# Optimization experiments

Hardware: AMD Instinct MI355X
Metric: run time of the kernel (lower is better)

## Reference

```python
import jax, jax.numpy as jnp
import numpy as np
import math

B, S, H, NS = 64, 1024, 1024, 8
TEMPERATURE = 1.0


def setup_inputs() -> dict:
    key = jax.random.key(0)
    ks = jax.random.split(key, 14)
    sc = 1.0 / math.sqrt(H)
    inp = {
        "x": jax.random.normal(ks[0], (B, S, H), dtype=jnp.float32),
        "Wq": jax.random.normal(ks[1], (H, H), dtype=jnp.float32) * sc,
        "bq": jax.random.normal(ks[2], (H,), dtype=jnp.float32) * sc,
        "Wk": jax.random.normal(ks[3], (H, H), dtype=jnp.float32) * sc,
        "bk": jax.random.normal(ks[4], (H,), dtype=jnp.float32) * sc,
        "Wv": jax.random.normal(ks[5], (H, H), dtype=jnp.float32) * sc,
        "bv": jax.random.normal(ks[6], (H,), dtype=jnp.float32) * sc,
        "Wp": jax.random.normal(ks[7], (NS, H, H), dtype=jnp.float32) * sc,
        "bp": jax.random.normal(ks[8], (NS, H), dtype=jnp.float32) * sc,
        "Ws": jax.random.normal(ks[9], (H, NS), dtype=jnp.float32) * sc,
        "bs": jax.random.normal(ks[10], (NS,), dtype=jnp.float32) * sc,
        "Wo": jax.random.normal(ks[11], (H, H), dtype=jnp.float32) * sc,
        "bo": jax.random.normal(ks[12], (H,), dtype=jnp.float32) * sc,
    }
    return inp


def reference(x, Wq, bq, Wk, bk, Wv, bv, Wp, bp, Ws, bs, Wo, bo):
    b, s_len, h = x.shape
    ns = Wp.shape[0]
    inv_base = 1.0 / math.sqrt(h * TEMPERATURE)
    inv_h = 1.0 / math.sqrt(h)

    x_last = x[:, -1, :]                      # [B,H]
    q = x_last @ Wq + bq                      # [B,H]
    k = x @ Wk + bk                           # [B,S,H]
    v = x @ Wv + bv                           # [B,S,H]

    attn_base = jax.nn.softmax(jnp.einsum("bh,bsh->bs", q, k) * inv_base, axis=-1)
    base_context = jnp.einsum("bs,bsh->bh", attn_base, v)   # [B,H]

    scale_importance = jax.nn.softmax(x_last @ Ws + bs, axis=-1)  # [B,NS]

    combined = jnp.zeros((b, h), dtype=x.dtype)
    for i in range(ns):
        size = max(1, s_len // (2 ** i))
        if size == 1:
            pooled = jnp.mean(x, axis=1, keepdims=True)      # [B,1,H]
        else:
            stride = max(1, size // 2)
            # S divisible by stride; window j = halves j and j+1
            half_sums = x.reshape(b, s_len // stride, stride, h).sum(axis=2)
            pooled = (half_sums[:, :-1] + half_sums[:, 1:]) / size  # [B,nw,H]
        feat = jnp.tanh(pooled @ Wp[i] + bp[i])              # [B,nw,H]
        fa = jax.nn.softmax(jnp.einsum("bh,bnh->bn", q, feat) * inv_h, axis=-1)
        ctx = jnp.einsum("bn,bnh->bh", fa, feat)
        combined = combined + scale_importance[:, i:i + 1] * ctx

    return (base_context + combined) @ Wo + bo
```

## Files before the change

kernel.cpp:

```cpp
#include <hip/hip_runtime.h>
#include <cstdint>
#include <cstddef>

#define BB 64
#define SS 1024
#define HH 1024
#define NSS 8

__device__ __constant__ int PBrow_c[8]    = {0,128,384,896,1920,3968,8064,16256};
__device__ __constant__ int realbase_c[8] = {0,64,256,704,1664,3648,7680,15808};

#define INV32 0.03125f

typedef __attribute__((ext_vector_type(8))) short short8;
typedef __attribute__((ext_vector_type(4))) float f32x4;

__device__ __forceinline__ uint16_t f2bf(float f) {
  union { float f; uint32_t u; } v; v.f = f;
  uint32_t r = v.u + 0x7fffu + ((v.u >> 16) & 1u);
  return (uint16_t)(r >> 16);
}
__device__ __forceinline__ float bf_lo(uint32_t w) { return __uint_as_float(w << 16); }
__device__ __forceinline__ float bf_hi(uint32_t w) { return __uint_as_float(w & 0xffff0000u); }

__device__ __forceinline__ void gld_lds16(const void* g, void* l) {
  __builtin_amdgcn_global_load_lds((const __attribute__((address_space(1))) uint32_t*)g,
                                   (__attribute__((address_space(3))) uint32_t*)l, 16, 0, 0);
}

template<bool TRANSB>
__global__ __launch_bounds__(256) void gemm64(
    const float* __restrict__ A, size_t a_stride,
    const float* __restrict__ W,
    const float* __restrict__ bias,
    const float* __restrict__ addb,
    float* __restrict__ out)
{
  __shared__ float As[64][68];
  __shared__ float Bs[64][68];
  const int t  = threadIdx.x;
  const int nt = blockIdx.x;
  const int ks = blockIdx.y;
  const int m0 = (t >> 4) << 2;
  const int n0 = (t & 15) << 2;
  float acc[4][4] = {};
  for (int kt = 0; kt < 4; ++kt) {
    const int k0 = ks * 256 + kt * 64;
    {
      const int m  = t >> 2;
      const int kb = (t & 3) << 4;
      #pragma unroll
      for (int j = 0; j < 4; ++j) {
        const int k = kb + j * 4;
        const float4 v = *(const float4*)(A + (size_t)m * a_stride + k0 + k);
        As[k+0][m] = v.x; As[k+1][m] = v.y; As[k+2][m] = v.z; As[k+3][m] = v.w;
      }
    }
    if (!TRANSB) {
      const int k  = t >> 2;
      const int nb = (t & 3) << 4;
      #pragma unroll
      for (int j = 0; j < 4; ++j) {
        const int n = nb + j * 4;
        *(float4*)&Bs[k][n] = *(const float4*)(W + (size_t)(k0 + k) * HH + nt * 64 + n);
      }
    } else {
      const int n  = t >> 2;
      const int kb = (t & 3) << 4;
      #pragma unroll
      for (int j = 0; j < 4; ++j) {
        const int k = kb + j * 4;
        const float4 v = *(const float4*)(W + (size_t)(nt * 64 + n) * HH + k0 + k);
        Bs[k+0][n] = v.x; Bs[k+1][n] = v.y; Bs[k+2][n] = v.z; Bs[k+3][n] = v.w;
      }
    }
    __syncthreads();
    #pragma unroll 16
    for (int k = 0; k < 64; ++k) {
      const float4 av = *(const float4*)&As[k][m0];
      const float4 bv = *(const float4*)&Bs[k][n0];
      const float a[4] = {av.x, av.y, av.z, av.w};
      const float b[4] = {bv.x, bv.y, bv.z, bv.w};
      #pragma unroll
      for (int i2 = 0; i2 < 4; ++i2)
        #pragma unroll
        for (int j2 = 0; j2 < 4; ++j2)
          acc[i2][j2] += a[i2] * b[j2];
    }
    __syncthreads();
  }
  #pragma unroll
  for (int i2 = 0; i2 < 4; ++i2) {
    const int m = m0 + i2;
    #pragma unroll
    for (int j2 = 0; j2 < 4; ++j2) {
      const int n = nt * 64 + n0 + j2;
      float v = acc[i2][j2];
      if (ks == 0) {
        if (bias) v += bias[n];
        if (addb) v += addb[(size_t)m * HH + n];
      }
      atomicAdd(out + (size_t)m * HH + n, v);
    }
  }
}

__global__ __launch_bounds__(256) void si_kernel(const float* __restrict__ x,
    const float* __restrict__ Ws, const float* __restrict__ bs,
    float* __restrict__ si)
{
  const int b = blockIdx.x, t = threadIdx.x;
  const int n = t & 7, kc = t >> 3;
  const float* xl = x + ((size_t)b * SS + (SS - 1)) * HH;
  float p = 0.f;
  for (int kk = 0; kk < 32; ++kk) {
    const int k = kc * 32 + kk;
    p += xl[k] * Ws[k * NSS + n];
  }
  __shared__ float red[32][9];
  __shared__ float lg[8];
  red[kc][n] = p;
  __syncthreads();
  if (t < 8) {
    float s2 = bs[t];
    for (int c = 0; c < 32; ++c) s2 += red[c][t];
    lg[t] = s2;
  }
  __syncthreads();
  if (t == 0) {
    float mx = lg[0];
    #pragma unroll
    for (int j = 1; j < 8; ++j) mx = fmaxf(mx, lg[j]);
    float e[8]; float sm = 0.f;
    #pragma unroll
    for (int j = 0; j < 8; ++j) { e[j] = expf(lg[j] - mx); sm += e[j]; }
    const float inv = 1.0f / sm;
    #pragma unroll
    for (int j = 0; j < 8; ++j) si[b * NSS + j] = e[j] * inv;
  }
}

__global__ __launch_bounds__(256) void score_kernel(const float* __restrict__ x,
    const float* __restrict__ qk, float* __restrict__ attn)
{
  const int b = blockIdx.y, sc = blockIdx.x;
  const int t = threadIdx.x;
  const int lane = t & 63, w = t >> 6;
  __shared__ float qks[HH];
  __shared__ float red[8][4];
  *(float4*)&qks[t * 4] = *(const float4*)&qk[b * HH + t * 4];
  __syncthreads();
  for (int ss = 0; ss < 8; ++ss) {
    const int s = sc * 8 + ss;
    const float4 xv = *(const float4*)&x[((size_t)b * SS + s) * HH + t * 4];
    const float4 qv = *(const float4*)&qks[t * 4];
    float p = xv.x * qv.x + xv.y * qv.y + xv.z * qv.z + xv.w * qv.w;
    #pragma unroll
    for (int off = 32; off > 0; off >>= 1) p += __shfl_down(p, off);
    if (lane == 0) red[ss][w] = p;
  }
  __syncthreads();
  if (t < 8) {
    const float v = (red[t][0] + red[t][1] + red[t][2] + red[t][3]) * INV32;
    attn[(size_t)b * SS + sc * 8 + t] = v;
  }
}

__global__ __launch_bounds__(256) void softmax_s(float* __restrict__ attn)
{
  const int b = blockIdx.x, t = threadIdx.x;
  float* row = attn + (size_t)b * SS;
  float4 v = *(float4*)&row[t * 4];
  float mx = fmaxf(fmaxf(v.x, v.y), fmaxf(v.z, v.w));
  #pragma unroll
  for (int off = 32; off > 0; off >>= 1) mx = fmaxf(mx, __shfl_xor(mx, off));
  __shared__ float rm[4];
  __shared__ float rs[4];
  if ((t & 63) == 0) rm[t >> 6] = mx;
  __syncthreads();
  mx = fmaxf(fmaxf(rm[0], rm[1]), fmaxf(rm[2], rm[3]));
  const float e0 = expf(v.x - mx), e1 = expf(v.y - mx), e2 = expf(v.z - mx), e3 = expf(v.w - mx);
  float sm = e0 + e1 + e2 + e3;
  #pragma unroll
  for (int off = 32; off > 0; off >>= 1) sm += __shfl_xor(sm, off);
  if ((t & 63) == 0) rs[t >> 6] = sm;
  __syncthreads();
  sm = rs[0] + rs[1] + rs[2] + rs[3];
  const float inv = 1.0f / sm;
  v.x = e0 * inv; v.y = e1 * inv; v.z = e2 * inv; v.w = e3 * inv;
  *(float4*)&row[t * 4] = v;
}

__global__ __launch_bounds__(256) void pool_kernel(const float* __restrict__ x,
    const float* __restrict__ attn, uint16_t* __restrict__ P,
    float* __restrict__ xa)
{
  const int b = blockIdx.y;
  const int h = blockIdx.x * 256 + threadIdx.x;
  __shared__ float at[SS];
  #pragma unroll
  for (int j = 0; j < 4; ++j) at[threadIdx.x + j * 256] = attn[(size_t)b * SS + threadIdx.x + j * 256];
  __syncthreads();
  const float* xp = x + (size_t)b * SS * HH + h;
  float lacc[8] = {0,0,0,0,0,0,0,0};
  float lprev[8] = {0,0,0,0,0,0,0,0};
  float xacc = 0.f, chunk = 0.f;
  for (int s8 = 0; s8 < 128; ++s8) {
    float v[8];
    #pragma unroll
    for (int j = 0; j < 8; ++j) v[j] = xp[(size_t)(s8 * 8 + j) * HH];
    #pragma unroll
    for (int j = 0; j < 8; ++j) {
      const int s = s8 * 8 + j;
      xacc += at[s] * v[j];
      chunk += v[j];
      if ((j & 3) == 3) {
        const int cidx = s >> 2;
        const float c = chunk; chunk = 0.f;
        #pragma unroll
        for (int L = 0; L < 8; ++L) {
          lacc[L] += c;
          if (((cidx + 1) & ((1 << L) - 1)) == 0) {
            const int mh = ((cidx + 1) >> L) - 1;
            if (mh >= 1) {
              const int i  = 7 - L;
              const int ni = (256 >> L) - 1;
              const int row = PBrow_c[i] + b * ni + (mh - 1);
              const float inv_size = 1.0f / (float)(8 << L);
              P[(size_t)row * HH + h] = f2bf((lprev[L] + lacc[L]) * inv_size);
            }
            lprev[L] = lacc[L]; lacc[L] = 0.f;
          }
        }
      }
    }
  }
  xa[(size_t)b * HH + h] = xacc;
}

__global__ __launch_bounds__(256) void wcvt(const float* __restrict__ Wp,
                                            uint16_t* __restrict__ WpT)
{
  __shared__ float tile[32][33];
  const int s = blockIdx.z;
  const int n0 = blockIdx.x * 32, k0 = blockIdx.y * 32;
  const float* src = Wp + (size_t)s * HH * HH;
  uint16_t* dst = WpT + (size_t)s * HH * HH;
  const int t = threadIdx.x;
  #pragma unroll
  for (int i = 0; i < 4; ++i) {
    const int kl = i * 8 + (t >> 5), nl = t & 31;
    tile[kl][nl] = src[(size_t)(k0 + kl) * HH + n0 + nl];
  }
  __syncthreads();
  #pragma unroll
  for (int i = 0; i < 4; ++i) {
    const int nl = i * 8 + (t >> 5), kl = t & 31;
    dst[(size_t)(n0 + nl) * HH + k0 + kl] = f2bf(tile[kl][nl]);
  }
}

__global__ __launch_bounds__(256) void feat_gemm(const uint16_t* __restrict__ P,
    const uint16_t* __restrict__ WpT, const float* __restrict__ bp,
    uint16_t* __restrict__ feat)
{
  __shared__ __align__(16) uint16_t As[4 * 128 * 8];
  __shared__ __align__(16) uint16_t Bs[4 * 128 * 8];
  const int t = threadIdx.x;
  const int w = t >> 6, lane = t & 63;
  const int quad = lane >> 4, l16 = lane & 15;
  const int ty = blockIdx.y;
  const int scale = 31 - __clz(ty + 1);
  const int tloc  = ty - ((1 << scale) - 1);
  const int row0  = PBrow_c[scale] + tloc * 128;
  const uint16_t* Wps = WpT + (size_t)scale * HH * HH;
  const float* bps = bp + scale * HH;
  const int ncol0 = blockIdx.x * 128;
  const int wm = (w & 1) * 64, wn = (w >> 1) * 64;

  f32x4 acc[4][4];
  #pragma unroll
  for (int mt = 0; mt < 4; ++mt)
    #pragma unroll
    for (int nt = 0; nt < 4; ++nt)
      acc[mt][nt] = (f32x4){0.f, 0.f, 0.f, 0.f};

  for (int k0 = 0; k0 < HH; k0 += 32) {
    #pragma unroll
    for (int i = w; i < 8; i += 4) {
      const int khalf = i >> 1, r0 = (i & 1) * 64;
      gld_lds16(P + (size_t)(row0 + r0 + lane) * HH + k0 + khalf * 8,
                As + (size_t)i * 512);
      gld_lds16(Wps + (size_t)(ncol0 + r0 + lane) * HH + k0 + khalf * 8,
                Bs + (size_t)i * 512);
    }
    __syncthreads();
    short8 af[4], bf[4];
    const short8* Asv = (const short8*)As;
    const short8* Bsv = (const short8*)Bs;
    #pragma unroll
    for (int mt = 0; mt < 4; ++mt) af[mt] = Asv[quad * 128 + wm + mt * 16 + l16];
    #pragma unroll
    for (int nt = 0; nt < 4; ++nt) bf[nt] = Bsv[quad * 128 + wn + nt * 16 + l16];
    #pragma unroll
    for (int mt = 0; mt < 4; ++mt)
      #pragma unroll
      for (int nt = 0; nt < 4; ++nt)
        acc[mt][nt] = __builtin_amdgcn_mfma_f32_16x16x32_bf16(af[mt], bf[nt], acc[mt][nt], 0, 0, 0);
    __syncthreads();
  }

  #pragma unroll
  for (int nt = 0; nt < 4; ++nt) {
    const int col = ncol0 + wn + nt * 16 + l16;
    const float bpv = bps[col];
    #pragma unroll
    for (int mt = 0; mt < 4; ++mt) {
      #pragma unroll
      for (int r = 0; r < 4; ++r) {
        const int row = row0 + wm + mt * 16 + quad * 4 + r;
        feat[(size_t)row * HH + col] = f2bf(tanhf(acc[mt][nt][r] + bpv));
      }
    }
  }
}

__global__ __launch_bounds__(256) void falogit_kernel(const uint16_t* __restrict__ feat,
    const float* __restrict__ q, float* __restrict__ l)
{
  const int w = threadIdx.x >> 6, lane = threadIdx.x & 63;
  const int r = blockIdx.x * 4 + w;
  int sc = 0;
  #pragma unroll
  for (int i = 1; i < 8; ++i) if (r >= realbase_c[i]) sc = i;
  const int local = r - realbase_c[sc];
  const int ni = (2 << sc) - 1;
  const int b = local / ni;
  const int prow = PBrow_c[sc] + local;
  const uint16_t* fr = feat + (size_t)prow * HH + lane * 16;
  const float*    qr = q + (size_t)b * HH + lane * 16;
  const uint4 f0 = *(const uint4*)fr;
  const uint4 f1 = *(const uint4*)(fr + 8);
  const float4 q0 = *(const float4*)(qr + 0);
  const float4 q1 = *(const float4*)(qr + 4);
  const float4 q2 = *(const float4*)(qr + 8);
  const float4 q3 = *(const float4*)(qr + 12);
  const uint32_t uf[8] = {f0.x, f0.y, f0.z, f0.w, f1.x, f1.y, f1.z, f1.w};
  const float qv[16] = {q0.x,q0.y,q0.z,q0.w, q1.x,q1.y,q1.z,q1.w,
                        q2.x,q2.y,q2.z,q2.w, q3.x,q3.y,q3.z,q3.w};
  float p = 0.f;
  #pragma unroll
  for (int j = 0; j < 8; ++j) {
    p += bf_lo(uf[j]) * qv[2 * j];
    p += bf_hi(uf[j]) * qv[2 * j + 1];
  }
  #pragma unroll
  for (int off = 32; off > 0; off >>= 1) p += __shfl_down(p, off);
  if (lane == 0) l[prow] = p * INV32;
}

__global__ __launch_bounds__(256) void ctx_kernel(const uint16_t* __restrict__ feat,
    const float* __restrict__ l, const float* __restrict__ si,
    float* __restrict__ comb)
{
  const int i = blockIdx.x, b = blockIdx.y, t = threadIdx.x;
  const int ni = (2 << i) - 1;
  const int base = PBrow_c[i] + b * ni;
  __shared__ float fa[256];
  __shared__ float rbuf[4];
  const float lg = (t < ni) ? l[base + t] : -1e30f;
  float mx = lg;
  #pragma unroll
  for (int off = 32; off > 0; off >>= 1) mx = fmaxf(mx, __shfl_xor(mx, off));
  if ((t & 63) == 0) rbuf[t >> 6] = mx;
  __syncthreads();
  mx = fmaxf(fmaxf(rbuf[0], rbuf[1]), fmaxf(rbuf[2], rbuf[3]));
  const float e = (t < ni) ? expf(lg - mx) : 0.f;
  float sm = e;
  #pragma unroll
  for (int off = 32; off > 0; off >>= 1) sm += __shfl_xor(sm, off);
  __syncthreads();
  if ((t & 63) == 0) rbuf[t >> 6] = sm;
  __syncthreads();
  sm = rbuf[0] + rbuf[1] + rbuf[2] + rbuf[3];
  fa[t] = e / sm;
  __syncthreads();
  float c0 = 0.f, c1 = 0.f, c2 = 0.f, c3 = 0.f;
  const int hb = t * 4;
  for (int n = 0; n < ni; ++n) {
    const float fn = fa[n];
    const uint2 u = *(const uint2*)(feat + (size_t)(base + n) * HH + hb);
    c0 += fn * bf_lo(u.x);
    c1 += fn * bf_hi(u.x);
    c2 += fn * bf_lo(u.y);
    c3 += fn * bf_hi(u.y);
  }
  const float sw = si[b * NSS + i];
  atomicAdd(&comb[(size_t)b * HH + hb + 0], sw * c0);
  atomicAdd(&comb[(size_t)b * HH + hb + 1], sw * c1);
  atomicAdd(&comb[(size_t)b * HH + hb + 2], sw * c2);
  atomicAdd(&comb[(size_t)b * HH + hb + 3], sw * c3);
}

extern "C" void kernel_launch(void* const* d_in, const int* in_sizes, int n_in,
                              void* d_out, int out_size, void* d_ws, size_t ws_size,
                              hipStream_t stream) {
  (void)in_sizes; (void)n_in; (void)out_size; (void)ws_size;
  const float* x  = (const float*)d_in[0];
  const float* Wq = (const float*)d_in[1];
  const float* bq = (const float*)d_in[2];
  const float* Wk = (const float*)d_in[3];
  const float* Wv = (const float*)d_in[5];
  const float* bv = (const float*)d_in[6];
  const float* Wp = (const float*)d_in[7];
  const float* bp = (const float*)d_in[8];
  const float* Ws = (const float*)d_in[9];
  const float* bs = (const float*)d_in[10];
  const float* Wo = (const float*)d_in[11];
  const float* bo = (const float*)d_in[12];
  float* out = (float*)d_out;
  char* ws = (char*)d_ws;

  const size_t P_BYTES   = (size_t)32640 * HH * 2;
  const size_t WPT_BYTES = (size_t)NSS * HH * HH * 2;
  uint16_t* P    = (uint16_t*)ws;
  uint16_t* feat = (uint16_t*)(ws + P_BYTES);
  uint16_t* WpT  = (uint16_t*)(ws + 2 * P_BYTES);
  float* q    = (float*)(ws + 2 * P_BYTES + WPT_BYTES);
  float* qk   = q    + (size_t)BB * HH;
  float* comb = qk   + (size_t)BB * HH;
  float* D    = comb + (size_t)BB * HH;
  float* attn = D    + (size_t)BB * HH;
  float* xa   = attn + (size_t)BB * SS;
  float* si   = xa   + (size_t)BB * HH;
  float* l    = si   + (size_t)BB * NSS;

  hipMemsetAsync(q, 0, (size_t)4 * BB * HH * sizeof(float), stream);
  hipMemsetAsync(d_out, 0, (size_t)BB * HH * sizeof(float), stream);

  wcvt<<<dim3(32, 32, NSS), 256, 0, stream>>>(Wp, WpT);
  gemm64<false><<<dim3(16, 4), 256, 0, stream>>>(x + (size_t)(SS - 1) * HH, (size_t)SS * HH, Wq, bq, nullptr, q);
  si_kernel<<<BB, 256, 0, stream>>>(x, Ws, bs, si);
  gemm64<true><<<dim3(16, 4), 256, 0, stream>>>(q, (size_t)HH, Wk, nullptr, nullptr, qk);
  score_kernel<<<dim3(128, BB), 256, 0, stream>>>(x, qk, attn);
  softmax_s<<<BB, 256, 0, stream>>>(attn);
  pool_kernel<<<dim3(4, BB), 256, 0, stream>>>(x, attn, P, xa);
  feat_gemm<<<dim3(8, 255), 256, 0, stream>>>(P, WpT, bp, feat);
  falogit_kernel<<<8032, 256, 0, stream>>>(feat, q, l);
  ctx_kernel<<<dim3(NSS, BB), 256, 0, stream>>>(feat, l, si, comb);
  gemm64<false><<<dim3(16, 4), 256, 0, stream>>>(xa, (size_t)HH, Wv, bv, comb, D);
  gemm64<false><<<dim3(16, 4), 256, 0, stream>>>(D, (size_t)HH, Wo, bo, nullptr, out);
}
```

Measured before the change: 859.6 us.

## Store pooled rows and Wp in tiled packed layout for contiguous GEMM tile loads

The pooling kernel and the Wp conversion kernel now write the bf16 operands in a blocked layout of 128 rows by 64 k-columns, grouped into 8-element chunks. Each GEMM k-step can then load a whole tile with fully contiguous 16-byte global-to-LDS loads instead of strided row gathers. The k-step grows from 32 to 64, so LDS tiles double and there are half as many barrier pairs. The pooling loop is also unrolled to 16 loads per iteration, which adds register pressure. Scattered writes in pool and wcvt may cost more.

```diff
diff --git a/kernel.cpp b/kernel.cpp
--- a/kernel.cpp
+++ b/kernel.cpp
@@ -26,6 +26,11 @@
 __device__ __forceinline__ void gld_lds16(const void* g, void* l) {
   __builtin_amdgcn_global_load_lds((const __attribute__((address_space(1))) uint32_t*)g,
                                    (__attribute__((address_space(3))) uint32_t*)l, 16, 0, 0);
+}
+
+__device__ __forceinline__ size_t pk_idx(int row, int k) {
+  return (((size_t)(row >> 7) * 16 + (k >> 6)) * 8 + ((k >> 3) & 7)) * 1024
+         + (size_t)(row & 127) * 8 + (k & 7);
 }
 
 template<bool TRANSB>
@@ -205,13 +210,13 @@
   float lacc[8] = {0,0,0,0,0,0,0,0};
   float lprev[8] = {0,0,0,0,0,0,0,0};
   float xacc = 0.f, chunk = 0.f;
-  for (int s8 = 0; s8 < 128; ++s8) {
-    float v[8];
-    #pragma unroll
-    for (int j = 0; j < 8; ++j) v[j] = xp[(size_t)(s8 * 8 + j) * HH];
-    #pragma unroll
-    for (int j = 0; j < 8; ++j) {
-      const int s = s8 * 8 + j;
+  for (int s16 = 0; s16 < 64; ++s16) {
+    float v[16];
+    #pragma unroll
+    for (int j = 0; j < 16; ++j) v[j] = xp[(size_t)(s16 * 16 + j) * HH];
+    #pragma unroll
+    for (int j = 0; j < 16; ++j) {
+      const int s = s16 * 16 + j;
       xacc += at[s] * v[j];
       chunk += v[j];
       if ((j & 3) == 3) {
@@ -227,7 +232,7 @@
               const int ni = (256 >> L) - 1;
               const int row = PBrow_c[i] + b * ni + (mh - 1);
               const float inv_size = 1.0f / (float)(8 << L);
-              P[(size_t)row * HH + h] = f2bf((lprev[L] + lacc[L]) * inv_size);
+              P[pk_idx(row, h)] = f2bf((lprev[L] + lacc[L]) * inv_size);
             }
             lprev[L] = lacc[L]; lacc[L] = 0.f;
           }
@@ -239,13 +244,13 @@
 }
 
 __global__ __launch_bounds__(256) void wcvt(const float* __restrict__ Wp,
-                                            uint16_t* __restrict__ WpT)
+                                            uint16_t* __restrict__ Wpk)
 {
   __shared__ float tile[32][33];
   const int s = blockIdx.z;
   const int n0 = blockIdx.x * 32, k0 = blockIdx.y * 32;
   const float* src = Wp + (size_t)s * HH * HH;
-  uint16_t* dst = WpT + (size_t)s * HH * HH;
+  uint16_t* dst = Wpk + (size_t)s * HH * HH;
   const int t = threadIdx.x;
   #pragma unroll
   for (int i = 0; i < 4; ++i) {
@@ -256,16 +261,16 @@
   #pragma unroll
   for (int i = 0; i < 4; ++i) {
     const int nl = i * 8 + (t >> 5), kl = t & 31;
-    dst[(size_t)(n0 + nl) * HH + k0 + kl] = f2bf(tile[kl][nl]);
+    dst[pk_idx(n0 + nl, k0 + kl)] = f2bf(tile[kl][nl]);
   }
 }
 
 __global__ __launch_bounds__(256) void feat_gemm(const uint16_t* __restrict__ P,
-    const uint16_t* __restrict__ WpT, const float* __restrict__ bp,
+    const uint16_t* __restrict__ Wpk, const float* __restrict__ bp,
     uint16_t* __restrict__ feat)
 {
-  __shared__ __align__(16) uint16_t As[4 * 128 * 8];
-  __shared__ __align__(16) uint16_t Bs[4 * 128 * 8];
+  __shared__ __align__(16) uint16_t As[8 * 128 * 8];
+  __shared__ __align__(16) uint16_t Bs[8 * 128 * 8];
   const int t = threadIdx.x;
   const int w = t >> 6, lane = t & 63;
   const int quad = lane >> 4, l16 = lane & 15;
@@ -273,9 +278,10 @@
   const int scale = 31 - __clz(ty + 1);
   const int tloc  = ty - ((1 << scale) - 1);
   const int row0  = PBrow_c[scale] + tloc * 128;
-  const uint16_t* Wps = WpT + (size_t)scale * HH * HH;
+  const int rt    = row0 >> 7;
+  const int ct    = blockIdx.x;
   const float* bps = bp + scale * HH;
-  const int ncol0 = blockIdx.x * 128;
+  const int ncol0 = ct * 128;
   const int wm = (w & 1) * 64, wn = (w >> 1) * 64;
 
   f32x4 acc[4][4];
@@ -285,28 +291,31 @@
     for (int nt = 0; nt < 4; ++nt)
       acc[mt][nt] = (f32x4){0.f, 0.f, 0.f, 0.f};
 
-  for (int k0 = 0; k0 < HH; k0 += 32) {
-    #pragma unroll
-    for (int i = w; i < 8; i += 4) {
-      const int khalf = i >> 1, r0 = (i & 1) * 64;
-      gld_lds16(P + (size_t)(row0 + r0 + lane) * HH + k0 + khalf * 8,
-                As + (size_t)i * 512);
-      gld_lds16(Wps + (size_t)(ncol0 + r0 + lane) * HH + k0 + khalf * 8,
-                Bs + (size_t)i * 512);
+  const short8* Asv = (const short8*)As;
+  const short8* Bsv = (const short8*)Bs;
+
+  for (int kb2 = 0; kb2 < 16; ++kb2) {
+    const uint16_t* Ag = P   + ((size_t)(rt * 16 + kb2)) * 8192;
+    const uint16_t* Bg = Wpk + ((size_t)((scale * 8 + ct) * 16 + kb2)) * 8192;
+    #pragma unroll
+    for (int i = w; i < 16; i += 4) {
+      gld_lds16(Ag + i * 512 + lane * 8, As + i * 512);
+      gld_lds16(Bg + i * 512 + lane * 8, Bs + i * 512);
     }
     __syncthreads();
-    short8 af[4], bf[4];
-    const short8* Asv = (const short8*)As;
-    const short8* Bsv = (const short8*)Bs;
-    #pragma unroll
-    for (int mt = 0; mt < 4; ++mt) af[mt] = Asv[quad * 128 + wm + mt * 16 + l16];
-    #pragma unroll
-    for (int nt = 0; nt < 4; ++nt) bf[nt] = Bsv[quad * 128 + wn + nt * 16 + l16];
-    #pragma unroll
-    for (int mt = 0; mt < 4; ++mt)
-      #pragma unroll
-      for (int nt = 0; nt < 4; ++nt)
-        acc[mt][nt] = __builtin_amdgcn_mfma_f32_16x16x32_bf16(af[mt], bf[nt], acc[mt][nt], 0, 0, 0);
+    #pragma unroll
+    for (int ks2 = 0; ks2 < 2; ++ks2) {
+      short8 af[4], bf[4];
+      #pragma unroll
+      for (int mt = 0; mt < 4; ++mt) af[mt] = Asv[(ks2 * 4 + quad) * 128 + wm + mt * 16 + l16];
+      #pragma unroll
+      for (int nt = 0; nt < 4; ++nt) bf[nt] = Bsv[(ks2 * 4 + quad) * 128 + wn + nt * 16 + l16];
+      #pragma unroll
+      for (int mt = 0; mt < 4; ++mt)
+        #pragma unroll
+        for (int nt = 0; nt < 4; ++nt)
+          acc[mt][nt] = __builtin_amdgcn_mfma_f32_16x16x32_bf16(af[mt], bf[nt], acc[mt][nt], 0, 0, 0);
+    }
     __syncthreads();
   }
 
@@ -425,7 +434,7 @@
   const size_t WPT_BYTES = (size_t)NSS * HH * HH * 2;
   uint16_t* P    = (uint16_t*)ws;
   uint16_t* feat = (uint16_t*)(ws + P_BYTES);
-  uint16_t* WpT  = (uint16_t*)(ws + 2 * P_BYTES);
+  uint16_t* Wpk  = (uint16_t*)(ws + 2 * P_BYTES);
   float* q    = (float*)(ws + 2 * P_BYTES + WPT_BYTES);
   float* qk   = q    + (size_t)BB * HH;
   float* comb = qk   + (size_t)BB * HH;
@@ -438,14 +447,14 @@
   hipMemsetAsync(q, 0, (size_t)4 * BB * HH * sizeof(float), stream);
   hipMemsetAsync(d_out, 0, (size_t)BB * HH * sizeof(float), stream);
 
-  wcvt<<<dim3(32, 32, NSS), 256, 0, stream>>>(Wp, WpT);
+  wcvt<<<dim3(32, 32, NSS), 256, 0, stream>>>(Wp, Wpk);
   gemm64<false><<<dim3(16, 4), 256, 0, stream>>>(x + (size_t)(SS - 1) * HH, (size_t)SS * HH, Wq, bq, nullptr, q);
   si_kernel<<<BB, 256, 0, stream>>>(x, Ws, bs, si);
   gemm64<true><<<dim3(16, 4), 256, 0, stream>>>(q, (size_t)HH, Wk, nullptr, nullptr, qk);
   score_kernel<<<dim3(128, BB), 256, 0, stream>>>(x, qk, attn);
   softmax_s<<<BB, 256, 0, stream>>>(attn);
   pool_kernel<<<dim3(4, BB), 256, 0, stream>>>(x, attn, P, xa);
-  feat_gemm<<<dim3(8, 255), 256, 0, stream>>>(P, WpT, bp, feat);
+  feat_gemm<<<dim3(8, 255), 256, 0, stream>>>(P, Wpk, bp, feat);
   falogit_kernel<<<8032, 256, 0, stream>>>(feat, q, l);
   ctx_kernel<<<dim3(NSS, BB), 256, 0, stream>>>(feat, l, si, comb);
   gemm64<false><<<dim3(16, 4), 256, 0, stream>>>(xa, (size_t)HH, Wv, bv, comb, D);
```

After: 786.6 us. 8.5% less time.
